# Optimization experiments

Measured on AMD Instinct MI355X. Metric: run time of the kernel, lower is better.

The kernel has to match this reference:

```python
import jax, jax.numpy as jnp
import numpy as np

PATCH = 14

def _patchify(t, p):
    # (B,C,H,W) -> (B*pH*pW, C, p*p)
    B, C, H, W = t.shape
    pH, pW = H // p, W // p
    t = t.reshape(B, C, pH, p, pW, p).transpose(0, 2, 4, 1, 3, 5)
    return t.reshape(B * pH * pW, C, p * p)

def _unpatchify(t, B, C, H, W, p):
    pH, pW = H // p, W // p
    t = t.reshape(B, pH, pW, C, p, p).transpose(0, 3, 1, 4, 2, 5)
    return t.reshape(B, C, H, W)

def setup_inputs() -> dict:
    key = jax.random.key(0)
    ks = jax.random.split(key, 9)
    B, C, H, W = 4, 256, 224, 224
    s = 1.0 / np.sqrt(C)
    return {
        "x": jax.random.normal(ks[0], (B, C, H, W), jnp.float32),
        "skip0": jax.random.normal(ks[1], (B, C, 112, 112), jnp.float32),
        "skip1": jax.random.normal(ks[2], (B, C, 56, 56), jnp.float32),
        "Wq": jax.random.normal(ks[3], (C, C), jnp.float32) * s,
        "bq": jax.random.normal(ks[4], (C,), jnp.float32) * 0.01,
        "Wk": jax.random.normal(ks[5], (C, C), jnp.float32) * s,
        "bk": jax.random.normal(ks[6], (C,), jnp.float32) * 0.01,
        "Wv": jax.random.normal(ks[7], (C, C), jnp.float32) * s,
        "bv": jax.random.normal(ks[8], (C,), jnp.float32) * 0.01,
    }

def reference(x, skip0, skip1, Wq, bq, Wk, bk, Wv, bv):
    B, C, H, W = x.shape
    p = PATCH
    xp = _patchify(x, p)                       # (N, C, L), L = p*p
    # 1x1 conv on x (query) is shared across skips
    Q = jnp.einsum('oc,ncl->nol', Wq, xp) + bq[None, :, None]
    out = 0.0
    for skip in (skip0, skip1):
        sk = jax.image.resize(skip, (B, C, H, W), method='bilinear')  # align_corners=False
        sp = _patchify(sk, p)
        K = jnp.einsum('oc,ncl->nol', Wk, sp) + bk[None, :, None]
        V = jnp.einsum('oc,ncl->nol', Wv, sp) + bv[None, :, None]
        attn = jax.nn.softmax(jnp.einsum('ncl,ncm->nlm', Q, K), axis=-1)  # unscaled, per original
        out = out + jnp.einsum('nlm,ncm->ncl', attn, V)
    return _unpatchify(out, B, C, H, W, p)
```

## Files before the change

kernel.cpp:

```cpp
#include <hip/hip_runtime.h>

typedef _Float16 f16;
typedef _Float16 f16x8 __attribute__((ext_vector_type(8)));
typedef float f32x4 __attribute__((ext_vector_type(4)));

#define DEV static __device__ __forceinline__

constexpr int  NPATCH = 1024;
constexpr int  LLEN   = 196;
constexpr long NLROWS = (long)NPATCH * LLEN;

DEV void g2l16(const void* g, void* l) {
  __builtin_amdgcn_global_load_lds(
      (const __attribute__((address_space(1))) unsigned int*)g,
      (__attribute__((address_space(3))) unsigned int*)l, 16, 0, 0);
}

__global__ __launch_bounds__(256) void k0_prep(
    const float* __restrict__ Wq, const float* __restrict__ Wk,
    const float* __restrict__ Wv, const float* __restrict__ bq,
    f16* __restrict__ G16, f16* __restrict__ Wv16, float* __restrict__ u32) {
  int bx = blockIdx.x, t = threadIdx.x;
  if (bx < 256) {
    int c = bx;
    float acc = 0.f;
    for (int o = 0; o < 256; ++o) acc += Wq[o*256 + c] * Wk[o*256 + t];
    G16[c*256 + t] = (f16)acc;
  } else if (bx == 256) {
    float acc = 0.f;
    for (int o = 0; o < 256; ++o) acc += bq[o] * Wk[o*256 + t];
    u32[t] = acc;
  } else {
    for (int r = 0; r < 256; ++r) Wv16[r*256 + t] = (f16)Wv[r*256 + t];
  }
}

__global__ __launch_bounds__(256) void k1_pack(
    const float* __restrict__ src, int Hs, int Ws, float invS,
    f16* __restrict__ dst, float* __restrict__ ub,
    const float* __restrict__ u32, int do_ub) {
  __shared__ float tile[224 * 65];
  __shared__ float us[64];
  int bx = blockIdx.x;
  int cc0 = (bx & 3) * 64;
  int bi = bx >> 2;
  int i  = bi % 14; bi /= 14;
  int py = bi & 15; int b = bi >> 4;
  int y = py*14 + i;
  float fy  = (y + 0.5f) * invS - 0.5f;
  float y0f = floorf(fy);
  float wy1 = fy - y0f, wy0 = 1.f - wy1;
  int y0 = (int)y0f, y1 = (int)y0f + 1;
  y0 = min(max(y0, 0), Hs-1); y1 = min(max(y1, 0), Hs-1);
  int t = threadIdx.x;
  if (t < 64) us[t] = u32[cc0 + t];
  int xl = t & 63, c4 = t >> 6;
  for (int xp = 0; xp < 4; ++xp) {
    int x = xp*64 + xl;
    if (x < 224) {
      float fx  = (x + 0.5f) * invS - 0.5f;
      float x0f = floorf(fx);
      float wx1 = fx - x0f, wx0 = 1.f - wx1;
      int x0 = (int)x0f, x1 = (int)x0f + 1;
      x0 = min(max(x0, 0), Ws-1); x1 = min(max(x1, 0), Ws-1);
      for (int co = 0; co < 16; ++co) {
        int c = cc0 + co*4 + c4;
        const float* base = src + ((long)(b*256 + c) * Hs) * Ws;
        float v;
        if (invS == 1.0f) {
          v = base[y0*Ws + x0];
        } else {
          float v00 = base[y0*Ws + x0], v01 = base[y0*Ws + x1];
          float v10 = base[y1*Ws + x0], v11 = base[y1*Ws + x1];
          v = wy0*(wx0*v00 + wx1*v01) + wy1*(wx0*v10 + wx1*v11);
        }
        tile[x*65 + co*4 + c4] = v;
      }
    }
  }
  __syncthreads();
  int cp = t & 31, xg = t >> 5;
  float u0 = us[2*cp], u1 = us[2*cp + 1];
  for (int xo = 0; xo < 28; ++xo) {
    int x = xo*8 + xg;
    float v0 = tile[x*65 + 2*cp], v1 = tile[x*65 + 2*cp + 1];
    int px = x / 14, j = x % 14;
    int m = i*14 + j;
    long nm = (long)(b*256 + py*16 + px) * 196 + m;
    union { f16 h[2]; unsigned uu; } pk;
    pk.h[0] = (f16)v0; pk.h[1] = (f16)v1;
    *(unsigned*)(dst + nm*256 + cc0 + 2*cp) = pk.uu;
    if (do_ub) {
      float part = u0*v0 + u1*v1;
      part += __shfl_xor(part, 1);
      part += __shfl_xor(part, 2);
      part += __shfl_xor(part, 4);
      part += __shfl_xor(part, 8);
      part += __shfl_xor(part, 16);
      if (cp == 0) atomicAdd(ub + nm, part);
    }
  }
}

__global__ __launch_bounds__(256) void k2_kv(
    const f16* __restrict__ SPT, const f16* __restrict__ G16,
    const f16* __restrict__ Wv16, f16* __restrict__ KtT, f16* __restrict__ VT2) {
  __shared__ __align__(16) char ldsA[64 * 80];
  __shared__ __align__(16) char ldsB[512 * 80];
  int tid = threadIdx.x;
  int lane = tid & 63, wv = tid >> 6;
  long nm0 = (long)blockIdx.x * 64;
  f32x4 zero = {0.f, 0.f, 0.f, 0.f};
  f32x4 acc[4][8];
#pragma unroll
  for (int a = 0; a < 4; ++a)
#pragma unroll
    for (int bb = 0; bb < 8; ++bb) acc[a][bb] = zero;
  int col0 = wv * 128;
  int r15 = lane & 15, quad = lane >> 4;
  for (int k0 = 0; k0 < 256; k0 += 32) {
    __syncthreads();
#pragma unroll
    for (int call = 0; call < 2; ++call) {
      int slot = call*256 + tid;
      if (slot < 320) {
        int row = slot / 5, part = slot % 5;
        int pp_ = part < 4 ? part : 0;
        g2l16(SPT + ((nm0 + row)*256 + k0 + pp_*8), ldsA + slot*16);
      }
    }
#pragma unroll
    for (int call = 0; call < 10; ++call) {
      int slot = call*256 + tid;
      int row = slot / 5, part = slot % 5;
      int pp_ = part < 4 ? part : 0;
      const f16* g = (row < 256) ? (G16 + (row*256 + k0 + pp_*8))
                                 : (Wv16 + ((row - 256)*256 + k0 + pp_*8));
      g2l16(g, ldsB + slot*16);
    }
    __syncthreads();
    f16x8 af[4];
#pragma unroll
    for (int rt = 0; rt < 4; ++rt)
      af[rt] = *(const f16x8*)(ldsA + (rt*16 + r15)*80 + quad*16);
#pragma unroll
    for (int tc = 0; tc < 8; ++tc) {
      f16x8 bf = *(const f16x8*)(ldsB + (col0 + tc*16 + r15)*80 + quad*16);
#pragma unroll
      for (int rt = 0; rt < 4; ++rt)
        acc[rt][tc] = __builtin_amdgcn_mfma_f32_16x16x32_f16(af[rt], bf, acc[rt][tc], 0, 0, 0);
    }
  }
  __syncthreads();
  f16* ldsV = (f16*)ldsB;
  if (wv >= 2) {
#pragma unroll
    for (int rt = 0; rt < 4; ++rt)
#pragma unroll
      for (int tc = 0; tc < 8; ++tc) {
        int o = col0 - 256 + tc*16 + r15;
#pragma unroll
        for (int reg = 0; reg < 4; ++reg) {
          int row = rt*16 + quad*4 + reg;
          ldsV[row*258 + o] = (f16)acc[rt][tc][reg];
        }
      }
  } else {
#pragma unroll
    for (int rt = 0; rt < 4; ++rt)
#pragma unroll
      for (int tc = 0; tc < 8; ++tc) {
        int colc = col0 + tc*16 + r15;
#pragma unroll
        for (int reg = 0; reg < 4; ++reg) {
          long row = nm0 + rt*16 + quad*4 + reg;
          KtT[row*256 + colc] = (f16)acc[rt][tc][reg];
        }
      }
  }
  __syncthreads();
  {
    int row = tid & 63;
    long nm = nm0 + row;
    int n = (int)(nm / 196), m = (int)(nm % 196);
    long vbase = ((long)n * 256) * 224 + m;
    int o0 = (tid >> 6) * 64;
    for (int it = 0; it < 64; ++it) {
      int o = o0 + it;
      VT2[vbase + (long)o * 224] = ldsV[row*258 + o];
    }
  }
}

__global__ __launch_bounds__(256) void k3_s(
    const f16* __restrict__ XT, const f16* __restrict__ KtT,
    const float* __restrict__ ub, f16* __restrict__ Pout) {
  __shared__ __align__(16) char ldsA[64 * 144];
  __shared__ __align__(16) char ldsB[208 * 144];
  __shared__ float ubs[208];
  int tid = threadIdx.x;
  int lane = tid & 63, wv = tid >> 6;
  int bx = blockIdx.x;
  int n  = ((bx >> 5) << 3) | (bx & 7);
  int l0 = ((bx >> 3) & 3) * 64;
  long base = (long)n * 196;
  for (int s = tid; s < 208; s += 256) ubs[s] = (s < 196) ? ub[base + s] : 0.f;
  f32x4 zero = {0.f, 0.f, 0.f, 0.f};
  f32x4 acc[13];
#pragma unroll
  for (int t = 0; t < 13; ++t) acc[t] = zero;
  int r15 = lane & 15, quad = lane >> 4;
  for (int k0 = 0; k0 < 256; k0 += 64) {
    __syncthreads();
#pragma unroll
    for (int call = 0; call < 3; ++call) {
      int slot = call*256 + tid;
      if (slot < 576) {
        int row = slot / 9, part = slot % 9;
        int pp_ = part < 8 ? part : 0;
        int l = l0 + row; l = l > 195 ? 195 : l;
        g2l16(XT + ((base + l)*256 + k0 + pp_*8), ldsA + slot*16);
      }
    }
#pragma unroll
    for (int call = 0; call < 8; ++call) {
      int slot = call*256 + tid;
      if (slot < 1872) {
        int row = slot / 9, part = slot % 9;
        int pp_ = part < 8 ? part : 0;
        int m = row > 195 ? 195 : row;
        g2l16(KtT + ((base + m)*256 + k0 + pp_*8), ldsB + slot*16);
      }
    }
    __syncthreads();
#pragma unroll
    for (int ks = 0; ks < 2; ++ks) {
      f16x8 af = *(const f16x8*)(ldsA + (wv*16 + r15)*144 + (ks*4 + quad)*16);
#pragma unroll
      for (int t = 0; t < 13; ++t) {
        f16x8 bf = *(const f16x8*)(ldsB + (t*16 + r15)*144 + (ks*4 + quad)*16);
        acc[t] = __builtin_amdgcn_mfma_f32_16x16x32_f16(af, bf, acc[t], 0, 0, 0);
      }
    }
  }
  float mx[4] = {-1e30f, -1e30f, -1e30f, -1e30f};
#pragma unroll
  for (int t = 0; t < 13; ++t) {
    int colb = t*16 + r15;
    float ubv = ubs[colb];
    bool valid = colb < 196;
#pragma unroll
    for (int reg = 0; reg < 4; ++reg) {
      float v = acc[t][reg] + ubv;
      acc[t][reg] = v;
      if (valid) mx[reg] = fmaxf(mx[reg], v);
    }
  }
#pragma unroll
  for (int reg = 0; reg < 4; ++reg) {
    float m = mx[reg];
    m = fmaxf(m, __shfl_xor(m, 1));
    m = fmaxf(m, __shfl_xor(m, 2));
    m = fmaxf(m, __shfl_xor(m, 4));
    m = fmaxf(m, __shfl_xor(m, 8));
    mx[reg] = m;
  }
  float sum[4] = {0.f, 0.f, 0.f, 0.f};
#pragma unroll
  for (int t = 0; t < 13; ++t) {
    int colb = t*16 + r15;
    bool valid = colb < 196;
#pragma unroll
    for (int reg = 0; reg < 4; ++reg) {
      float p = valid ? __expf(acc[t][reg] - mx[reg]) : 0.f;
      acc[t][reg] = p;
      sum[reg] += p;
    }
  }
#pragma unroll
  for (int reg = 0; reg < 4; ++reg) {
    float s = sum[reg];
    s += __shfl_xor(s, 1);
    s += __shfl_xor(s, 2);
    s += __shfl_xor(s, 4);
    s += __shfl_xor(s, 8);
    sum[reg] = 1.0f / s;
  }
#pragma unroll
  for (int reg = 0; reg < 4; ++reg) {
    int l = l0 + wv*16 + quad*4 + reg;
    if (l < 196) {
      long prow = (base + l) * 224;
#pragma unroll
      for (int t = 0; t < 13; ++t)
        Pout[prow + t*16 + r15] = (f16)(acc[t][reg] * sum[reg]);
      Pout[prow + 208 + r15] = (f16)0.f;
    }
  }
}

__global__ __launch_bounds__(256) void k4_o(
    const f16* __restrict__ Pbuf, const f16* __restrict__ VT2,
    f16* __restrict__ Obuf, int mode) {
  __shared__ __align__(16) char ldsA[64 * 80];
  __shared__ __align__(16) char ldsB[256 * 80];
  int tid = threadIdx.x;
  int lane = tid & 63, wv = tid >> 6;
  int bx = blockIdx.x;
  int n  = ((bx >> 5) << 3) | (bx & 7);
  int l0 = ((bx >> 3) & 3) * 64;
  f32x4 zero = {0.f, 0.f, 0.f, 0.f};
  f32x4 acc[16];
#pragma unroll
  for (int t = 0; t < 16; ++t) acc[t] = zero;
  int r15 = lane & 15, quad = lane >> 4;
  for (int m0 = 0; m0 < 224; m0 += 32) {
    __syncthreads();
#pragma unroll
    for (int call = 0; call < 2; ++call) {
      int slot = call*256 + tid;
      if (slot < 320) {
        int row = slot / 5, part = slot % 5;
        int pp_ = part < 4 ? part : 0;
        long nl = (long)n*196 + l0 + row;
        if (nl > NLROWS - 1) nl = NLROWS - 1;
        g2l16(Pbuf + (nl*224 + m0 + pp_*8), ldsA + slot*16);
      }
    }
#pragma unroll
    for (int call = 0; call < 5; ++call) {
      int slot = call*256 + tid;
      int row = slot / 5, part = slot % 5;
      int pp_ = part < 4 ? part : 0;
      g2l16(VT2 + (((long)(n*256 + row))*224 + m0 + pp_*8), ldsB + slot*16);
    }
    __syncthreads();
    f16x8 af = *(const f16x8*)(ldsA + (wv*16 + r15)*80 + quad*16);
#pragma unroll
    for (int t = 0; t < 16; ++t) {
      f16x8 bf = *(const f16x8*)(ldsB + (t*16 + r15)*80 + quad*16);
      acc[t] = __builtin_amdgcn_mfma_f32_16x16x32_f16(af, bf, acc[t], 0, 0, 0);
    }
  }
#pragma unroll
  for (int reg = 0; reg < 4; ++reg) {
    int l = l0 + wv*16 + quad*4 + reg;
    if (l < 196) {
      long orow = ((long)n*196 + l) * 256;
#pragma unroll
      for (int t = 0; t < 16; ++t) {
        int c = t*16 + r15;
        float v = acc[t][reg];
        if (mode == 0) Obuf[orow + c] = (f16)v;
        else           Obuf[orow + c] = (f16)(v + (float)Obuf[orow + c]);
      }
    }
  }
}

__global__ __launch_bounds__(256) void k5_unpatch(
    const f16* __restrict__ Obuf, const float* __restrict__ bv,
    float* __restrict__ out) {
  __shared__ float lds[64 * 225];
  int bx = blockIdx.x;
  int cc = (bx & 3) * 64;  bx >>= 2;
  int i  = bx % 14; bx /= 14;
  int py = bx & 15; int b = bx >> 4;
  int t = threadIdx.x;
  int cl = t & 63, pg = t >> 6;
  for (int it = 0; it < 56; ++it) {
    int pr = it*4 + pg;
    int px = pr / 14, j = pr % 14;
    int n = b*256 + py*16 + px;
    float v = (float)Obuf[((long)n*196 + i*14 + j)*256 + cc + cl];
    lds[cl*225 + px*14 + j] = v;
  }
  __syncthreads();
  int yy = py*14 + i;
  for (int c = 0; c < 64; ++c) {
    float bb = 2.0f * bv[cc + c];
    if (t < 224)
      out[(((long)(b*256 + cc + c))*224 + yy)*224 + t] = lds[c*225 + t] + bb;
  }
}

extern "C" void kernel_launch(void* const* d_in, const int* in_sizes, int n_in,
                              void* d_out, int out_size, void* d_ws, size_t ws_size,
                              hipStream_t stream) {
  (void)in_sizes; (void)n_in; (void)out_size; (void)ws_size;
  const float* x     = (const float*)d_in[0];
  const float* skip0 = (const float*)d_in[1];
  const float* skip1 = (const float*)d_in[2];
  const float* Wq    = (const float*)d_in[3];
  const float* bq    = (const float*)d_in[4];
  const float* Wk    = (const float*)d_in[5];
  const float* Wv    = (const float*)d_in[7];
  const float* bv    = (const float*)d_in[8];
  float* out = (float*)d_out;

  char* ws = (char*)d_ws;
  size_t off = 0;
  auto alloc = [&](size_t bytes) {
    char* p = ws + off;
    off += (bytes + 255) & ~(size_t)255;
    return p;
  };
  f16*   XT   = (f16*)  alloc((size_t)NLROWS * 256 * 2);
  f16*   SPT  = (f16*)  alloc((size_t)NLROWS * 256 * 2);
  f16*   KtT  = (f16*)  alloc((size_t)NLROWS * 256 * 2);
  f16*   VT2  = (f16*)  alloc((size_t)NPATCH * 256 * 224 * 2);
  f16*   Obuf = (f16*)  alloc((size_t)NLROWS * 256 * 2);
  float* ub   = (float*)alloc((size_t)NLROWS * 4);
  f16*   G16  = (f16*)  alloc(256 * 256 * 2);
  f16*   Wv16 = (f16*)  alloc(256 * 256 * 2);
  float* u32  = (float*)alloc(256 * 4);
  f16*   P    = SPT;

  k0_prep<<<258, 256, 0, stream>>>(Wq, Wk, Wv, bq, G16, Wv16, u32);
  k1_pack<<<3584, 256, 0, stream>>>(x, 224, 224, 1.0f, XT, nullptr, u32, 0);

  const float* skips[2] = {skip0, skip1};
  int   hs[2]   = {112, 56};
  float invs[2] = {0.5f, 0.25f};
  for (int s = 0; s < 2; ++s) {
    hipMemsetAsync(ub, 0, (size_t)NLROWS * 4, stream);
    k1_pack<<<3584, 256, 0, stream>>>(skips[s], hs[s], hs[s], invs[s], SPT, ub, u32, 1);
    k2_kv<<<3136, 256, 0, stream>>>(SPT, G16, Wv16, KtT, VT2);
    k3_s <<<4096, 256, 0, stream>>>(XT, KtT, ub, P);
    k4_o <<<4096, 256, 0, stream>>>(P, VT2, Obuf, s);
  }
  k5_unpatch<<<3584, 256, 0, stream>>>(Obuf, bv, out);
}
```

Measured before the change: 1.879 ms.

## Vectorize pack kernel, replace ub atomics with partial sums, double-buffer PV GEMM

```diff
diff --git a/kernel.cpp b/kernel.cpp
--- a/kernel.cpp
+++ b/kernel.cpp
@@ -14,6 +14,12 @@
   __builtin_amdgcn_global_load_lds(
       (const __attribute__((address_space(1))) unsigned int*)g,
       (__attribute__((address_space(3))) unsigned int*)l, 16, 0, 0);
+}
+
+DEV unsigned pk2(float a, float b) {
+  union { f16 h[2]; unsigned u; } z;
+  z.h[0] = (f16)a; z.h[1] = (f16)b;
+  return z.u;
 }
 
 __global__ __launch_bounds__(256) void k0_prep(
@@ -37,9 +43,9 @@
 
 __global__ __launch_bounds__(256) void k1_pack(
     const float* __restrict__ src, int Hs, int Ws, float invS,
-    f16* __restrict__ dst, float* __restrict__ ub,
+    f16* __restrict__ dst, float* __restrict__ ub4,
     const float* __restrict__ u32, int do_ub) {
-  __shared__ float tile[224 * 65];
+  __shared__ unsigned tile[32 * 225];
   __shared__ float us[64];
   int bx = blockIdx.x;
   int cc0 = (bx & 3) * 64;
@@ -47,57 +53,84 @@
   int i  = bi % 14; bi /= 14;
   int py = bi & 15; int b = bi >> 4;
   int y = py*14 + i;
-  float fy  = (y + 0.5f) * invS - 0.5f;
-  float y0f = floorf(fy);
-  float wy1 = fy - y0f, wy0 = 1.f - wy1;
-  int y0 = (int)y0f, y1 = (int)y0f + 1;
-  y0 = min(max(y0, 0), Hs-1); y1 = min(max(y1, 0), Hs-1);
   int t = threadIdx.x;
   if (t < 64) us[t] = u32[cc0 + t];
-  int xl = t & 63, c4 = t >> 6;
-  for (int xp = 0; xp < 4; ++xp) {
-    int x = xp*64 + xl;
-    if (x < 224) {
-      float fx  = (x + 0.5f) * invS - 0.5f;
-      float x0f = floorf(fx);
-      float wx1 = fx - x0f, wx0 = 1.f - wx1;
-      int x0 = (int)x0f, x1 = (int)x0f + 1;
-      x0 = min(max(x0, 0), Ws-1); x1 = min(max(x1, 0), Ws-1);
-      for (int co = 0; co < 16; ++co) {
-        int c = cc0 + co*4 + c4;
-        const float* base = src + ((long)(b*256 + c) * Hs) * Ws;
-        float v;
-        if (invS == 1.0f) {
-          v = base[y0*Ws + x0];
-        } else {
-          float v00 = base[y0*Ws + x0], v01 = base[y0*Ws + x1];
-          float v10 = base[y1*Ws + x0], v11 = base[y1*Ws + x1];
-          v = wy0*(wx0*v00 + wx1*v01) + wy1*(wx0*v10 + wx1*v11);
+
+  if (invS == 1.0f) {
+    int xh = t & 7, pr = t >> 3;
+    const float* b0 = src + ((long)(b*256 + cc0 + 2*pr)) * 50176 + y*224;
+    const float* b1 = b0 + 50176;
+#pragma unroll
+    for (int it = 0; it < 7; ++it) {
+      int x0 = (it*8 + xh) * 4;
+      float4 va = *(const float4*)(b0 + x0);
+      float4 vb = *(const float4*)(b1 + x0);
+      tile[pr*225 + x0 + 0] = pk2(va.x, vb.x);
+      tile[pr*225 + x0 + 1] = pk2(va.y, vb.y);
+      tile[pr*225 + x0 + 2] = pk2(va.z, vb.z);
+      tile[pr*225 + x0 + 3] = pk2(va.w, vb.w);
+    }
+  } else {
+    float fy  = (y + 0.5f) * invS - 0.5f;
+    float y0f = floorf(fy);
+    float wy1 = fy - y0f, wy0 = 1.f - wy1;
+    int y0 = (int)y0f, y1 = (int)y0f + 1;
+    y0 = min(max(y0, 0), Hs-1); y1 = min(max(y1, 0), Hs-1);
+    long plane = (long)Hs * Ws;
+    int xl = t & 63, c4 = t >> 6;
+    for (int xp = 0; xp < 4; ++xp) {
+      int x = xp*64 + xl;
+      if (x < 224) {
+        float fx  = (x + 0.5f) * invS - 0.5f;
+        float x0f = floorf(fx);
+        float wx1 = fx - x0f, wx0 = 1.f - wx1;
+        int x0 = (int)x0f, x1 = (int)x0f + 1;
+        x0 = min(max(x0, 0), Ws-1); x1 = min(max(x1, 0), Ws-1);
+        int o00 = y0*Ws + x0, o01 = y0*Ws + x1;
+        int o10 = y1*Ws + x0, o11 = y1*Ws + x1;
+#pragma unroll
+        for (int pp = 0; pp < 8; ++pp) {
+          int pr = c4*8 + pp;
+          const float* base0 = src + ((long)(b*256 + cc0 + 2*pr)) * plane;
+          const float* base1 = base0 + plane;
+          float va = wy0*(wx0*base0[o00] + wx1*base0[o01])
+                   + wy1*(wx0*base0[o10] + wx1*base0[o11]);
+          float vb = wy0*(wx0*base1[o00] + wx1*base1[o01])
+                   + wy1*(wx0*base1[o10] + wx1*base1[o11]);
+          tile[pr*225 + x] = pk2(va, vb);
         }
-        tile[x*65 + co*4 + c4] = v;
       }
     }
   }
   __syncthreads();
-  int cp = t & 31, xg = t >> 5;
-  float u0 = us[2*cp], u1 = us[2*cp + 1];
-  for (int xo = 0; xo < 28; ++xo) {
-    int x = xo*8 + xg;
-    float v0 = tile[x*65 + 2*cp], v1 = tile[x*65 + 2*cp + 1];
+  int q = t & 7, xg = t >> 3;
+  float4 u0, u1;
+  if (do_ub) {
+    u0 = *(const float4*)(us + q*8);
+    u1 = *(const float4*)(us + q*8 + 4);
+  }
+  for (int xo = 0; xo < 7; ++xo) {
+    int x = xo*32 + xg;
+    unsigned p0 = tile[(q*4+0)*225 + x];
+    unsigned p1 = tile[(q*4+1)*225 + x];
+    unsigned p2 = tile[(q*4+2)*225 + x];
+    unsigned p3 = tile[(q*4+3)*225 + x];
     int px = x / 14, j = x % 14;
     int m = i*14 + j;
     long nm = (long)(b*256 + py*16 + px) * 196 + m;
-    union { f16 h[2]; unsigned uu; } pk;
-    pk.h[0] = (f16)v0; pk.h[1] = (f16)v1;
-    *(unsigned*)(dst + nm*256 + cc0 + 2*cp) = pk.uu;
+    uint4 w; w.x = p0; w.y = p1; w.z = p2; w.w = p3;
+    *reinterpret_cast<uint4*>(dst + nm*256 + cc0 + q*8) = w;
     if (do_ub) {
-      float part = u0*v0 + u1*v1;
+      union { unsigned u; f16 h[2]; } c0, c1, c2, c3;
+      c0.u = p0; c1.u = p1; c2.u = p2; c3.u = p3;
+      float part = u0.x*(float)c0.h[0] + u0.y*(float)c0.h[1]
+                 + u0.z*(float)c1.h[0] + u0.w*(float)c1.h[1]
+                 + u1.x*(float)c2.h[0] + u1.y*(float)c2.h[1]
+                 + u1.z*(float)c3.h[0] + u1.w*(float)c3.h[1];
       part += __shfl_xor(part, 1);
       part += __shfl_xor(part, 2);
       part += __shfl_xor(part, 4);
-      part += __shfl_xor(part, 8);
-      part += __shfl_xor(part, 16);
-      if (cp == 0) atomicAdd(ub + nm, part);
+      if (q == 0) ub4[(long)(bx & 3) * NLROWS + nm] = part;
     }
   }
 }
@@ -204,7 +237,14 @@
   int n  = ((bx >> 5) << 3) | (bx & 7);
   int l0 = ((bx >> 3) & 3) * 64;
   long base = (long)n * 196;
-  for (int s = tid; s < 208; s += 256) ubs[s] = (s < 196) ? ub[base + s] : 0.f;
+  for (int s = tid; s < 208; s += 256) {
+    float v = 0.f;
+    if (s < 196) {
+      long o = base + s;
+      v = ub[o] + ub[NLROWS + o] + ub[2*NLROWS + o] + ub[3*NLROWS + o];
+    }
+    ubs[s] = v;
+  }
   f32x4 zero = {0.f, 0.f, 0.f, 0.f};
   f32x4 acc[13];
 #pragma unroll
@@ -302,8 +342,8 @@
 __global__ __launch_bounds__(256) void k4_o(
     const f16* __restrict__ Pbuf, const f16* __restrict__ VT2,
     f16* __restrict__ Obuf, int mode) {
-  __shared__ __align__(16) char ldsA[64 * 80];
-  __shared__ __align__(16) char ldsB[256 * 80];
+  __shared__ __align__(16) char ldsA[2][64 * 80];
+  __shared__ __align__(16) char ldsB[2][256 * 80];
   int tid = threadIdx.x;
   int lane = tid & 63, wv = tid >> 6;
   int bx = blockIdx.x;
@@ -314,8 +354,8 @@
 #pragma unroll
   for (int t = 0; t < 16; ++t) acc[t] = zero;
   int r15 = lane & 15, quad = lane >> 4;
-  for (int m0 = 0; m0 < 224; m0 += 32) {
-    __syncthreads();
+
+  auto stage = [&](int buf, int m0) {
 #pragma unroll
     for (int call = 0; call < 2; ++call) {
       int slot = call*256 + tid;
@@ -324,7 +364,7 @@
         int pp_ = part < 4 ? part : 0;
         long nl = (long)n*196 + l0 + row;
         if (nl > NLROWS - 1) nl = NLROWS - 1;
-        g2l16(Pbuf + (nl*224 + m0 + pp_*8), ldsA + slot*16);
+        g2l16(Pbuf + (nl*224 + m0 + pp_*8), ldsA[buf] + slot*16);
       }
     }
 #pragma unroll
@@ -332,15 +372,22 @@
       int slot = call*256 + tid;
       int row = slot / 5, part = slot % 5;
       int pp_ = part < 4 ? part : 0;
-      g2l16(VT2 + (((long)(n*256 + row))*224 + m0 + pp_*8), ldsB + slot*16);
+      g2l16(VT2 + (((long)(n*256 + row))*224 + m0 + pp_*8), ldsB[buf] + slot*16);
+    }
+  };
+
+  stage(0, 0);
+  __syncthreads();
+  for (int it = 0; it < 7; ++it) {
+    int cur = it & 1;
+    if (it < 6) stage(cur ^ 1, 32*(it+1));
+    f16x8 af = *(const f16x8*)(ldsA[cur] + (wv*16 + r15)*80 + quad*16);
+#pragma unroll
+    for (int t = 0; t < 16; ++t) {
+      f16x8 bf = *(const f16x8*)(ldsB[cur] + (t*16 + r15)*80 + quad*16);
+      acc[t] = __builtin_amdgcn_mfma_f32_16x16x32_f16(af, bf, acc[t], 0, 0, 0);
     }
     __syncthreads();
-    f16x8 af = *(const f16x8*)(ldsA + (wv*16 + r15)*80 + quad*16);
-#pragma unroll
-    for (int t = 0; t < 16; ++t) {
-      f16x8 bf = *(const f16x8*)(ldsB + (t*16 + r15)*80 + quad*16);
-      acc[t] = __builtin_amdgcn_mfma_f32_16x16x32_f16(af, bf, acc[t], 0, 0, 0);
-    }
   }
 #pragma unroll
   for (int reg = 0; reg < 4; ++reg) {
@@ -410,7 +457,7 @@
   f16*   KtT  = (f16*)  alloc((size_t)NLROWS * 256 * 2);
   f16*   VT2  = (f16*)  alloc((size_t)NPATCH * 256 * 224 * 2);
   f16*   Obuf = (f16*)  alloc((size_t)NLROWS * 256 * 2);
-  float* ub   = (float*)alloc((size_t)NLROWS * 4);
+  float* ub   = (float*)alloc((size_t)NLROWS * 4 * 4);
   f16*   G16  = (f16*)  alloc(256 * 256 * 2);
   f16*   Wv16 = (f16*)  alloc(256 * 256 * 2);
   float* u32  = (float*)alloc(256 * 4);
@@ -423,7 +470,6 @@
   int   hs[2]   = {112, 56};
   float invs[2] = {0.5f, 0.25f};
   for (int s = 0; s < 2; ++s) {
-    hipMemsetAsync(ub, 0, (size_t)NLROWS * 4, stream);
     k1_pack<<<3584, 256, 0, stream>>>(skips[s], hs[s], hs[s], invs[s], SPT, ub, u32, 1);
     k2_kv<<<3136, 256, 0, stream>>>(SPT, G16, Wv16, KtT, VT2);
     k3_s <<<4096, 256, 0, stream>>>(XT, KtT, ub, P);
```

Result: faster. 1.709 ms (-9.0%).
